# Performance work log

Measured on AMD Instinct MI355X. Metric: run time of the kernel, lower is better.

## Reference

```python
import jax, jax.numpy as jnp
import numpy as np

B, S, D, H = 8, 1024, 768, 12
HS = D // H  # 64


def setup_inputs() -> dict:
    key = jax.random.key(0)
    k1, k2, k3 = jax.random.split(key, 3)
    x = jax.random.normal(k1, (B, S, D), dtype=jnp.float32)
    W_attn = jax.random.normal(k2, (D, 3 * H * HS), dtype=jnp.float32) * 0.02
    b_attn = jnp.zeros((3 * H * HS,), dtype=jnp.float32)
    W_proj = jax.random.normal(k3, (H * HS, D), dtype=jnp.float32) * 0.02
    b_proj = jnp.zeros((D,), dtype=jnp.float32)
    return {"x": x, "W_attn": W_attn, "b_attn": b_attn, "W_proj": W_proj, "b_proj": b_proj}


def reference(x, W_attn, b_attn, W_proj, b_proj):
    b, s, d = x.shape
    # qkv projection: [B,S,3*H*HS] -> [B,S,3,H,HS]
    qkv = (x @ W_attn + b_attn).reshape(b, s, 3, H, HS)
    q, k, v = qkv[:, :, 0], qkv[:, :, 1], qkv[:, :, 2]  # each [B,S,H,HS]
    scale = jnp.sqrt(jnp.asarray(HS, dtype=x.dtype))
    # scores: [B,H,Q,K]
    scores = jnp.einsum("bqhd,bkhd->bhqk", q, k) / scale
    causal = jnp.tril(jnp.ones((s, s), dtype=bool))  # [Q,K]
    scores = jnp.where(causal, scores, -jnp.inf)
    attn = jax.nn.softmax(scores, axis=-1)
    # dropout p=0.0 / inference -> identity
    out = jnp.einsum("bhqk,bkhd->bqhd", attn, v).reshape(b, s, H * HS)
    return out @ W_proj + b_proj
```

## Files before the change

kernel.cpp:

```cpp
#include <hip/hip_runtime.h>
#include <hip/hip_bf16.h>
#include <cstdint>
#include <cmath>

constexpr int B  = 8;
constexpr int S  = 1024;
constexpr int D  = 768;
constexpr int H  = 12;
constexpr int HS = 64;
constexpr int QKVN = 3 * D;

typedef __bf16 bf16x8 __attribute__((ext_vector_type(8)));
typedef float  f32x4  __attribute__((ext_vector_type(4)));

#define MFMA16(a, b, c) __builtin_amdgcn_mfma_f32_16x16x32_bf16((a), (b), (c), 0, 0, 0)

__device__ __forceinline__ void gl_lds16(const void* g, void* l) {
  __builtin_amdgcn_global_load_lds(
      (__attribute__((address_space(1))) void*)g,
      (__attribute__((address_space(3))) void*)l,
      16, 0, 0);
}

__global__ __launch_bounds__(256) void convert_f32_bf16(const float* __restrict__ in,
                                                        __bf16* __restrict__ out, int n) {
  int i = (blockIdx.x * 256 + threadIdx.x) * 8;
  if (i >= n) return;
  float4 f0 = *(const float4*)(in + i);
  float4 f1 = *(const float4*)(in + i + 4);
  bf16x8 o;
  o[0] = (__bf16)f0.x; o[1] = (__bf16)f0.y; o[2] = (__bf16)f0.z; o[3] = (__bf16)f0.w;
  o[4] = (__bf16)f1.x; o[5] = (__bf16)f1.y; o[6] = (__bf16)f1.z; o[7] = (__bf16)f1.w;
  *(bf16x8*)(out + i) = o;
}

__global__ __launch_bounds__(256) void transpose_w(const float* __restrict__ W,
                                                   __bf16* __restrict__ Wt,
                                                   int K, int N) {
  __shared__ float tile[64][65];
  const int n0 = blockIdx.x * 64, k0 = blockIdx.y * 64;
  const int t = threadIdx.x;
#pragma unroll
  for (int i = 0; i < 16; ++i) {
    int e = i * 256 + t;
    int r = e >> 6, c = e & 63;
    tile[r][c] = W[(size_t)(k0 + r) * N + n0 + c];
  }
  __syncthreads();
#pragma unroll
  for (int i = 0; i < 16; ++i) {
    int e = i * 256 + t;
    int r = e >> 6, c = e & 63;
    Wt[(size_t)(n0 + r) * K + k0 + c] = (__bf16)tile[c][r];
  }
}

__global__ __launch_bounds__(256) void build_vt(const __bf16* __restrict__ qkv,
                                                __bf16* __restrict__ Vt) {
  __shared__ __bf16 tile[64][65];
  const int s0 = blockIdx.x * 64;
  const int bh = blockIdx.y;
  const int b = bh / H, h = bh % H;
  const int t = threadIdx.x;
#pragma unroll
  for (int i = 0; i < 16; ++i) {
    int e = i * 256 + t;
    int r = e >> 6, c = e & 63;
    tile[r][c] = qkv[(size_t)(b * S + s0 + r) * QKVN + 2 * D + h * HS + c];
  }
  __syncthreads();
#pragma unroll
  for (int i = 0; i < 16; ++i) {
    int e = i * 256 + t;
    int r = e >> 6, c = e & 63;
    Vt[((size_t)(b * H + h) * HS + r) * S + s0 + c] = tile[c][r];
  }
}

template <typename CT>
__global__ __launch_bounds__(256) void gemm_bt(const __bf16* __restrict__ A,
                                               const __bf16* __restrict__ Bt,
                                               const float* __restrict__ bias,
                                               CT* __restrict__ C,
                                               int M, int N, int K) {
  __shared__ __bf16 As[128 * 32];
  __shared__ __bf16 Bs[128 * 32];
  const int t = threadIdx.x;
  const int w = t >> 6, l = t & 63, lr = l & 15, lg = l >> 4;
  const int wr = w >> 1, wc = w & 1;
  const int m0 = blockIdx.y * 128, n0 = blockIdx.x * 128;

  f32x4 acc[4][4] = {};

  for (int k0 = 0; k0 < K; k0 += 32) {
    __syncthreads();
#pragma unroll
    for (int i = 0; i < 2; ++i) {
      int e = i * 256 + t;
      int row = e >> 2;
      int cb = (e & 3) * 16;
      gl_lds16((const char*)(A + (size_t)(m0 + row) * K + k0) + cb, (char*)As + e * 16);
      gl_lds16((const char*)(Bt + (size_t)(n0 + row) * K + k0) + cb, (char*)Bs + e * 16);
    }
    asm volatile("s_waitcnt vmcnt(0)" ::: "memory");
    __syncthreads();

    bf16x8 a[4], bb[4];
#pragma unroll
    for (int mt = 0; mt < 4; ++mt)
      a[mt] = *(const bf16x8*)&As[(wr * 64 + mt * 16 + lr) * 32 + lg * 8];
#pragma unroll
    for (int nt = 0; nt < 4; ++nt)
      bb[nt] = *(const bf16x8*)&Bs[(wc * 64 + nt * 16 + lr) * 32 + lg * 8];
#pragma unroll
    for (int mt = 0; mt < 4; ++mt)
#pragma unroll
      for (int nt = 0; nt < 4; ++nt)
        acc[mt][nt] = MFMA16(a[mt], bb[nt], acc[mt][nt]);
  }

#pragma unroll
  for (int mt = 0; mt < 4; ++mt)
#pragma unroll
    for (int nt = 0; nt < 4; ++nt) {
#pragma unroll
      for (int r = 0; r < 4; ++r) {
        int row = m0 + wr * 64 + mt * 16 + lg * 4 + r;
        int col = n0 + wc * 64 + nt * 16 + lr;
        float v = acc[mt][nt][r] + bias[col];
        C[(size_t)row * N + col] = (CT)v;
      }
    }
}

__global__ __launch_bounds__(256, 3) void attn_kernel(const __bf16* __restrict__ qkv,
                                                      const __bf16* __restrict__ Vt,
                                                      __bf16* __restrict__ ao) {
  __shared__ __bf16 KV[2][2][64 * 64];
  __shared__ __bf16 Pb[2][4][16 * 64];

  const int t = threadIdx.x;
  const int w = t >> 6, l = t & 63, lr = l & 15, lg = l >> 4;
  const int qb = blockIdx.x;
  const int qA = qb, qB = 15 - qb;
  const int bh = blockIdx.y;
  const int b = bh / H, h = bh % H;
  const size_t qbase = (size_t)(b * S) * QKVN;

  const __bf16* Kg = qkv + qbase + D + h * HS;
  const __bf16* Vg = Vt + (size_t)(b * H + h) * HS * S;

  bf16x8 aqA[2], aqB[2];
  {
    const __bf16* qpA = qkv + qbase + (size_t)(qA * 64 + w * 16 + lr) * QKVN + h * HS + lg * 8;
    aqA[0] = *(const bf16x8*)qpA;
    aqA[1] = *(const bf16x8*)(qpA + 32);
    const __bf16* qpB = qkv + qbase + (size_t)(qB * 64 + w * 16 + lr) * QKVN + h * HS + lg * 8;
    aqB[0] = *(const bf16x8*)qpB;
    aqB[1] = *(const bf16x8*)(qpB + 32);
  }

  f32x4 oA[4] = {}, oB[4] = {};
  f32x4 lsA = {}, lsB = {};
  bf16x8 ones;
#pragma unroll
  for (int j = 0; j < 8; ++j) ones[j] = (__bf16)1.0f;

  const int xr = (lr & 7) << 3;
  const int nit = qB + 1;

  auto stage = [&](int buf, int it) {
    const int kv0 = it * 64;
#pragma unroll
    for (int i = 0; i < 2; ++i) {
      int e = i * 256 + t;
      int row = e >> 3;
      int cb = ((e & 7) * 16) ^ ((row & 7) << 4);
      gl_lds16((const char*)(Kg + (size_t)(kv0 + row) * QKVN) + cb,
               (char*)&KV[buf][0][0] + e * 16);
      gl_lds16((const char*)(Vg + (size_t)row * S + kv0) + cb,
               (char*)&KV[buf][1][0] + e * 16);
    }
  };

  stage(0, 0);
  asm volatile("s_waitcnt vmcnt(0)" ::: "memory");
  __syncthreads();

  const float SCL = 0.18033688011112042f;

  int cur = 0;
  for (int it = 0; it < nit; ++it) {
    if (it + 1 < nit) stage(cur ^ 1, it + 1);

    const __bf16* Ks = &KV[cur][0][0];
    const __bf16* Vs = &KV[cur][1][0];
    const bool doA = (it <= qA);

    f32x4 sA[4] = {}, sB[4] = {};
#pragma unroll
    for (int kk = 0; kk < 2; ++kk) {
      bf16x8 bk[4];
#pragma unroll
      for (int tc = 0; tc < 4; ++tc)
        bk[tc] = *(const bf16x8*)&Ks[(tc * 16 + lr) * 64 + ((kk * 32 + lg * 8) ^ xr)];
#pragma unroll
      for (int tc = 0; tc < 4; ++tc) sB[tc] = MFMA16(aqB[kk], bk[tc], sB[tc]);
      if (doA) {
#pragma unroll
        for (int tc = 0; tc < 4; ++tc) sA[tc] = MFMA16(aqA[kk], bk[tc], sA[tc]);
      }
    }

    __bf16* pwB = &Pb[1][w][0];
    {
      const bool dg = (it == qB);
#pragma unroll
      for (int tc = 0; tc < 4; ++tc)
#pragma unroll
        for (int r = 0; r < 4; ++r) {
          float v = sB[tc][r] * SCL;
          if (dg && (tc * 16 + lr) > (w * 16 + lg * 4 + r)) v = -INFINITY;
          float p = exp2f(v);
          int qrow = lg * 4 + r;
          pwB[qrow * 64 + ((tc * 16 + lr) ^ ((qrow & 7) << 3))] = (__bf16)p;
        }
    }
    __bf16* pwA = &Pb[0][w][0];
    if (doA) {
      const bool dg = (it == qA);
#pragma unroll
      for (int tc = 0; tc < 4; ++tc)
#pragma unroll
        for (int r = 0; r < 4; ++r) {
          float v = sA[tc][r] * SCL;
          if (dg && (tc * 16 + lr) > (w * 16 + lg * 4 + r)) v = -INFINITY;
          float p = exp2f(v);
          int qrow = lg * 4 + r;
          pwA[qrow * 64 + ((tc * 16 + lr) ^ ((qrow & 7) << 3))] = (__bf16)p;
        }
    }

#pragma unroll
    for (int kk = 0; kk < 2; ++kk) {
      bf16x8 apB = *(const bf16x8*)&pwB[lr * 64 + ((kk * 32 + lg * 8) ^ xr)];
      lsB = MFMA16(apB, ones, lsB);
      bf16x8 apA;
      if (doA) {
        apA = *(const bf16x8*)&pwA[lr * 64 + ((kk * 32 + lg * 8) ^ xr)];
        lsA = MFMA16(apA, ones, lsA);
      }
#pragma unroll
      for (int td = 0; td < 4; ++td) {
        bf16x8 bv = *(const bf16x8*)&Vs[(td * 16 + lr) * 64 + ((kk * 32 + lg * 8) ^ xr)];
        oB[td] = MFMA16(apB, bv, oB[td]);
        if (doA) oA[td] = MFMA16(apA, bv, oA[td]);
      }
    }

    asm volatile("s_waitcnt vmcnt(0)" ::: "memory");
    __syncthreads();
    cur ^= 1;
  }

#pragma unroll
  for (int r = 0; r < 4; ++r) {
    const float invA = 1.f / lsA[r];
    const float invB = 1.f / lsB[r];
    const int rowA = qA * 64 + w * 16 + lg * 4 + r;
    const int rowB = qB * 64 + w * 16 + lg * 4 + r;
#pragma unroll
    for (int td = 0; td < 4; ++td) {
      int col = h * HS + td * 16 + lr;
      ao[(size_t)(b * S + rowA) * D + col] = (__bf16)(oA[td][r] * invA);
      ao[(size_t)(b * S + rowB) * D + col] = (__bf16)(oB[td][r] * invB);
    }
  }
}

extern "C" void kernel_launch(void* const* d_in, const int* in_sizes, int n_in,
                              void* d_out, int out_size, void* d_ws, size_t ws_size,
                              hipStream_t stream) {
  const float* x      = (const float*)d_in[0];
  const float* W_attn = (const float*)d_in[1];
  const float* b_attn = (const float*)d_in[2];
  const float* W_proj = (const float*)d_in[3];
  const float* b_proj = (const float*)d_in[4];
  float* out = (float*)d_out;

  char* ws = (char*)d_ws;
  __bf16* xb  = (__bf16*)(ws + 0);
  __bf16* Wat = (__bf16*)(ws + 12582912);
  __bf16* Wpt = (__bf16*)(ws + 16121856);
  __bf16* qkv = (__bf16*)(ws + 17301504);
  __bf16* Vt  = (__bf16*)(ws + 55050240);
  __bf16* ao  = (__bf16*)(ws + 67633152);

  const int nX = B * S * D;

  convert_f32_bf16<<<nX / 8 / 256, 256, 0, stream>>>(x, xb, nX);
  transpose_w<<<dim3(QKVN / 64, D / 64), 256, 0, stream>>>(W_attn, Wat, D, QKVN);
  transpose_w<<<dim3(D / 64, D / 64), 256, 0, stream>>>(W_proj, Wpt, D, D);

  gemm_bt<__bf16><<<dim3(QKVN / 128, (B * S) / 128), 256, 0, stream>>>(
      xb, Wat, b_attn, qkv, B * S, QKVN, D);

  build_vt<<<dim3(S / 64, B * H), 256, 0, stream>>>(qkv, Vt);

  attn_kernel<<<dim3(8, B * H), 256, 0, stream>>>(qkv, Vt, ao);

  gemm_bt<float><<<dim3(D / 128, (B * S) / 128), 256, 0, stream>>>(
      ao, Wpt, b_proj, out, B * S, D, D);
}
```

Before: 204.3 us.

## Double-buffer GEMM LDS tiles, swizzle blocks across XCDs, add MFMA priority hints

The GEMM now double-buffers its A/B LDS tiles so the global-to-LDS load of the next K slice overlaps the MFMAs on the current one, at the cost of twice the shared memory. Both the GEMM and the attention kernel remap block IDs with an XCD swizzle, so neighbouring tiles that share operands land on the same XCD and its L2. The attention kernel also raises wave priority around its MFMA sections with s_setprio to interleave better with the softmax phases of other waves. The attention swizzle hard-codes 768 workgroups and assumes a grid of 8 by 96.

```diff
diff --git a/kernel.cpp b/kernel.cpp
--- a/kernel.cpp
+++ b/kernel.cpp
@@ -20,6 +20,11 @@
       (__attribute__((address_space(1))) void*)g,
       (__attribute__((address_space(3))) void*)l,
       16, 0, 0);
+}
+
+__device__ __forceinline__ int xcd_swizzle(int bid, int nwg) {
+  int chunk = nwg >> 3;
+  return (bid & 7) * chunk + (bid >> 3);
 }
 
 __global__ __launch_bounds__(256) void convert_f32_bf16(const float* __restrict__ in,
@@ -83,40 +88,54 @@
                                                const float* __restrict__ bias,
                                                CT* __restrict__ C,
                                                int M, int N, int K) {
-  __shared__ __bf16 As[128 * 32];
-  __shared__ __bf16 Bs[128 * 32];
+  __shared__ __bf16 As[2][128 * 32];
+  __shared__ __bf16 Bs[2][128 * 32];
   const int t = threadIdx.x;
   const int w = t >> 6, l = t & 63, lr = l & 15, lg = l >> 4;
   const int wr = w >> 1, wc = w & 1;
-  const int m0 = blockIdx.y * 128, n0 = blockIdx.x * 128;
+
+  const int nwg = gridDim.x * gridDim.y;
+  const int wg = xcd_swizzle(blockIdx.y * gridDim.x + blockIdx.x, nwg);
+  const int m0 = (wg / gridDim.x) * 128, n0 = (wg % gridDim.x) * 128;
 
   f32x4 acc[4][4] = {};
 
-  for (int k0 = 0; k0 < K; k0 += 32) {
-    __syncthreads();
+  auto stage = [&](int buf, int k0) {
 #pragma unroll
     for (int i = 0; i < 2; ++i) {
       int e = i * 256 + t;
       int row = e >> 2;
       int cb = (e & 3) * 16;
-      gl_lds16((const char*)(A + (size_t)(m0 + row) * K + k0) + cb, (char*)As + e * 16);
-      gl_lds16((const char*)(Bt + (size_t)(n0 + row) * K + k0) + cb, (char*)Bs + e * 16);
-    }
+      gl_lds16((const char*)(A + (size_t)(m0 + row) * K + k0) + cb, (char*)&As[buf][0] + e * 16);
+      gl_lds16((const char*)(Bt + (size_t)(n0 + row) * K + k0) + cb, (char*)&Bs[buf][0] + e * 16);
+    }
+  };
+
+  stage(0, 0);
+  asm volatile("s_waitcnt vmcnt(0)" ::: "memory");
+  __syncthreads();
+
+  const int nk = K / 32;
+  int cur = 0;
+  for (int kt = 0; kt < nk; ++kt) {
+    if (kt + 1 < nk) stage(cur ^ 1, (kt + 1) * 32);
+
+    bf16x8 a[4], bb[4];
+#pragma unroll
+    for (int mt = 0; mt < 4; ++mt)
+      a[mt] = *(const bf16x8*)&As[cur][(wr * 64 + mt * 16 + lr) * 32 + lg * 8];
+#pragma unroll
+    for (int nt = 0; nt < 4; ++nt)
+      bb[nt] = *(const bf16x8*)&Bs[cur][(wc * 64 + nt * 16 + lr) * 32 + lg * 8];
+#pragma unroll
+    for (int mt = 0; mt < 4; ++mt)
+#pragma unroll
+      for (int nt = 0; nt < 4; ++nt)
+        acc[mt][nt] = MFMA16(a[mt], bb[nt], acc[mt][nt]);
+
     asm volatile("s_waitcnt vmcnt(0)" ::: "memory");
     __syncthreads();
-
-    bf16x8 a[4], bb[4];
-#pragma unroll
-    for (int mt = 0; mt < 4; ++mt)
-      a[mt] = *(const bf16x8*)&As[(wr * 64 + mt * 16 + lr) * 32 + lg * 8];
-#pragma unroll
-    for (int nt = 0; nt < 4; ++nt)
-      bb[nt] = *(const bf16x8*)&Bs[(wc * 64 + nt * 16 + lr) * 32 + lg * 8];
-#pragma unroll
-    for (int mt = 0; mt < 4; ++mt)
-#pragma unroll
-      for (int nt = 0; nt < 4; ++nt)
-        acc[mt][nt] = MFMA16(a[mt], bb[nt], acc[mt][nt]);
+    cur ^= 1;
   }
 
 #pragma unroll
@@ -141,9 +160,11 @@
 
   const int t = threadIdx.x;
   const int w = t >> 6, l = t & 63, lr = l & 15, lg = l >> 4;
-  const int qb = blockIdx.x;
+
+  const int wg = xcd_swizzle(blockIdx.y * gridDim.x + blockIdx.x, 768);
+  const int qb = wg & 7;
+  const int bh = wg >> 3;
   const int qA = qb, qB = 15 - qb;
-  const int bh = blockIdx.y;
   const int b = bh / H, h = bh % H;
   const size_t qbase = (size_t)(b * S) * QKVN;
 
@@ -198,6 +219,7 @@
     const bool doA = (it <= qA);
 
     f32x4 sA[4] = {}, sB[4] = {};
+    __builtin_amdgcn_s_setprio(1);
 #pragma unroll
     for (int kk = 0; kk < 2; ++kk) {
       bf16x8 bk[4];
@@ -211,6 +233,7 @@
         for (int tc = 0; tc < 4; ++tc) sA[tc] = MFMA16(aqA[kk], bk[tc], sA[tc]);
       }
     }
+    __builtin_amdgcn_s_setprio(0);
 
     __bf16* pwB = &Pb[1][w][0];
     {
@@ -241,6 +264,7 @@
         }
     }
 
+    __builtin_amdgcn_s_setprio(1);
 #pragma unroll
     for (int kk = 0; kk < 2; ++kk) {
       bf16x8 apB = *(const bf16x8*)&pwB[lr * 64 + ((kk * 32 + lg * 8) ^ xr)];
@@ -257,6 +281,7 @@
         if (doA) oA[td] = MFMA16(apA, bv, oA[td]);
       }
     }
+    __builtin_amdgcn_s_setprio(0);
 
     asm volatile("s_waitcnt vmcnt(0)" ::: "memory");
     __syncthreads();
```

Measured after the change: 197.1 us. 3.5% less time.
